# Optimization experiments

Hardware: AMD Instinct MI355X
Metric: run time of the kernel (lower is better)

Reference implementation:

```python
import jax, jax.numpy as jnp
import numpy as np

N = 120_000      # points
D = 64           # voxel grid resolution per axis
HID = 96         # hidden_dim
IN = 96          # input_dim
C = HID + IN     # 192, conv input channels
EPS = 1e-5       # BatchNorm eps


def _build_geometry(rng):
    """Precompute the hash-map lookups torchsparse builds on the fly."""
    pts = rng.uniform(0, D - 1e-3, size=(N, 3)).astype(np.float32)
    vox = np.floor(pts).astype(np.int64)                      # voxel coord per point
    flat = (vox[:, 0] * D + vox[:, 1]) * D + vox[:, 2]
    uniq, seg = np.unique(flat, return_inverse=True)          # occupied voxels
    M = uniq.shape[0]
    lut = -np.ones(D * D * D, dtype=np.int64)
    lut[uniq] = np.arange(M)
    ux, uy, uz = uniq // (D * D), (uniq // D) % D, uniq % D
    # 27 kernel offsets for the 3x3x3 sparse conv
    offs = np.array([(dx, dy, dz) for dx in (-1, 0, 1)
                     for dy in (-1, 0, 1) for dz in (-1, 0, 1)], dtype=np.int64)
    nx = ux[:, None] + offs[None, :, 0]
    ny = uy[:, None] + offs[None, :, 1]
    nz = uz[:, None] + offs[None, :, 2]
    ok = (nx >= 0) & (nx < D) & (ny >= 0) & (ny < D) & (nz >= 0) & (nz < D)
    nflat = (np.clip(nx, 0, D - 1) * D + np.clip(ny, 0, D - 1)) * D + np.clip(nz, 0, D - 1)
    nbr = np.where(ok, lut[nflat], -1)
    nbr = np.where(nbr < 0, M, nbr).astype(np.int32)          # row M = zero pad
    # 8 trilinear corners for devoxelization
    frac = pts - vox
    coffs = np.array([(a, b, c) for a in (0, 1) for b in (0, 1) for c in (0, 1)], dtype=np.int64)
    cx = vox[:, 0:1] + coffs[None, :, 0]
    cy = vox[:, 1:2] + coffs[None, :, 1]
    cz = vox[:, 2:3] + coffs[None, :, 2]
    okc = (cx < D) & (cy < D) & (cz < D)
    cflat = (np.clip(cx, 0, D - 1) * D + np.clip(cy, 0, D - 1)) * D + np.clip(cz, 0, D - 1)
    cidx = np.where(okc, lut[cflat], -1)
    w = np.ones((N, 8), dtype=np.float32)
    for k in range(8):
        for d in range(3):
            w[:, k] *= frac[:, d] if coffs[k, d] == 1 else (1.0 - frac[:, d])
    w = np.where(cidx >= 0, w, 0.0).astype(np.float32)        # missing voxel -> weight 0
    cidx = np.where(cidx < 0, M, cidx).astype(np.int32)
    return seg.astype(np.int32), nbr, cidx, w


def setup_inputs() -> dict:
    rng = np.random.default_rng(0)
    seg, nbr, cidx, cw = _build_geometry(rng)
    key = jax.random.key(0)
    ks = jax.random.split(key, 4)
    return {
        "hidden_F": jax.random.normal(ks[0], (N, HID), jnp.float32),
        "query_F": jax.random.normal(ks[1], (N, IN), jnp.float32),
        "W_conv": jax.random.normal(ks[2], (27, C, HID), jnp.float32) * (1.0 / np.sqrt(27.0 * C)),
        "gamma": jnp.ones((HID,), jnp.float32),
        "beta": jnp.zeros((HID,), jnp.float32),
        "W_lin": jax.random.normal(ks[3], (C, IN), jnp.float32) * (1.0 / np.sqrt(C)),
        "b_lin": jnp.zeros((IN,), jnp.float32),
        "corner_w": jnp.asarray(cw),
        "seg_ids": jnp.asarray(seg),
        "nbr_idx": jnp.asarray(nbr),
        "corner_idx": jnp.asarray(cidx),
    }


def reference(hidden_F, query_F, W_conv, gamma, beta, W_lin, b_lin, corner_w,
              seg_ids, nbr_idx, corner_idx):
    M = nbr_idx.shape[0]
    hx = jnp.concatenate([hidden_F, query_F], axis=1)                  # [N, C]
    # initial_voxelize: scatter-mean point features into occupied voxels
    vsum = jax.ops.segment_sum(hx, seg_ids, num_segments=M)            # [M, C]
    cnt = jax.ops.segment_sum(jnp.ones((hx.shape[0], 1), hx.dtype),
                              seg_ids, num_segments=M)
    vfeat = vsum / jnp.maximum(cnt, 1.0)
    # sparse 3x3x3 conv: gather 27 hashed neighbors (row M is zero pad)
    vpad = jnp.concatenate([vfeat, jnp.zeros((1, C), vfeat.dtype)], axis=0)
    acc = jnp.zeros((M, HID), vfeat.dtype)
    for k in range(27):  # fixed small kernel loop
        acc = acc + vpad[nbr_idx[:, k]] @ W_conv[k]
    # BatchNorm (batch stats over occupied voxels) + ReLU
    mu = jnp.mean(acc, axis=0)
    var = jnp.mean((acc - mu) ** 2, axis=0)
    y = jax.nn.relu(gamma * (acc - mu) * jax.lax.rsqrt(var + EPS) + beta)
    # voxel_to_point(nearest=False): trilinear 8-corner gather
    ypad = jnp.concatenate([y, jnp.zeros((1, HID), y.dtype)], axis=0)
    out = jnp.zeros((hx.shape[0], HID), y.dtype)
    for k in range(8):  # fixed corner loop
        out = out + corner_w[:, k:k + 1] * ypad[corner_idx[:, k]]
    # residual point transform: out.F + Linear(hx.F)
    return out + hx @ W_lin + b_lin
```

## Files before the change

### kernel.cpp

```cpp
#include <hip/hip_runtime.h>
#include <hip/hip_bf16.h>
#include <cstdint>

typedef __bf16 bf16;
typedef __bf16 bf16x8 __attribute__((ext_vector_type(8)));
typedef __bf16 bf16x4 __attribute__((ext_vector_type(4)));
typedef float f32x4 __attribute__((ext_vector_type(4)));
typedef int i32x4 __attribute__((ext_vector_type(4)));

#define HIDC 96
#define CINC 192
#define EPSC 1e-5f

#define STG_B 20480
#define STG_ELEM 10240

#define GLD_LDS16(g, l)                                                        \
  __builtin_amdgcn_global_load_lds(                                            \
      (const __attribute__((address_space(1))) void*)(g),                      \
      (__attribute__((address_space(3))) void*)(l), 16, 0, 0)

__global__ void k_repack(const float* __restrict__ Wc, const float* __restrict__ Wl,
                         bf16* __restrict__ dst, int total) {
  int t = blockIdx.x * 256 + threadIdx.x;
  if (t >= total) return;
  int off = t / 18432;
  int rem = t - off * 18432;
  int cix = rem >> 9;
  int lane = (rem >> 3) & 63;
  int j = rem & 7;
  int k = (cix / 6) * 32 + ((lane >> 4) << 3) + j;
  int col = (cix % 6) * 16 + (lane & 15);
  const float* src = (off < 27) ? (Wc + ((size_t)off * CINC + k) * HIDC + col)
                                : (Wl + (size_t)k * HIDC + col);
  int half = (cix >= 18) ? 1 : 0;
  size_t de = (size_t)(off * 2 + half) * STG_ELEM + (size_t)(rem - half * 9216);
  dst[de] = (bf16)(*src);
}

__global__ void k_count(const int* __restrict__ seg, int* __restrict__ cnt, int Npts) {
  int t = blockIdx.x * 256 + threadIdx.x;
  if (t < Npts) atomicAdd(cnt + seg[t], 1);
}

__global__ void k_bsum(const int* __restrict__ cnt, int* __restrict__ bsum, int M) {
  __shared__ int sm[256];
  int i = blockIdx.x * 256 + threadIdx.x;
  sm[threadIdx.x] = (i < M) ? cnt[i] : 0;
  __syncthreads();
  for (int st = 128; st > 0; st >>= 1) {
    if (threadIdx.x < st) sm[threadIdx.x] += sm[threadIdx.x + st];
    __syncthreads();
  }
  if (threadIdx.x == 0) bsum[blockIdx.x] = sm[0];
}

__global__ void k_bscan(int* __restrict__ bsum, int nb) {
  __shared__ int sm[1024];
  int i = threadIdx.x;
  int v = (i < nb) ? bsum[i] : 0;
  sm[i] = v;
  __syncthreads();
  for (int st = 1; st < 1024; st <<= 1) {
    int t = (i >= st) ? sm[i - st] : 0;
    __syncthreads();
    sm[i] += t;
    __syncthreads();
  }
  if (i < nb) bsum[i] = sm[i] - v;
}

__global__ void k_ptr(const int* __restrict__ cnt, const int* __restrict__ bsum,
                      int* __restrict__ ptr, int* __restrict__ cursor, int M) {
  __shared__ int sm[256];
  int i = blockIdx.x * 256 + threadIdx.x;
  int v = (i < M) ? cnt[i] : 0;
  sm[threadIdx.x] = v;
  __syncthreads();
  for (int st = 1; st < 256; st <<= 1) {
    int t = (threadIdx.x >= st) ? sm[threadIdx.x - st] : 0;
    __syncthreads();
    sm[threadIdx.x] += t;
    __syncthreads();
  }
  if (i < M) {
    int e = bsum[blockIdx.x] + sm[threadIdx.x] - v;
    ptr[i] = e;
    cursor[i] = e;
  }
}

__global__ void k_scatter(const int* __restrict__ seg, int* __restrict__ cursor,
                          int* __restrict__ plist, int Npts) {
  int t = blockIdx.x * 256 + threadIdx.x;
  if (t < Npts) {
    int pos = atomicAdd(cursor + seg[t], 1);
    plist[pos] = t;
  }
}

__global__ void k_gmean(const float* __restrict__ hid, const float* __restrict__ qry,
                        const int* __restrict__ ptr, const int* __restrict__ cnt,
                        const int* __restrict__ plist, bf16* __restrict__ vpad, int M) {
  int t = blockIdx.x * 256 + threadIdx.x;
  if (t >= (M + 1) * 48) return;
  int v = t / 48;
  int q = t - v * 48;
  f32x4 a = {0.f, 0.f, 0.f, 0.f};
  if (v < M) {
    int st = ptr[v], n = cnt[v];
    const float* base = (q < 24) ? (hid + q * 4) : (qry + (q - 24) * 4);
    for (int j = 0; j < n; j++) {
      int p = plist[st + j];
      a += *(const f32x4*)(base + (size_t)p * HIDC);
    }
    a *= (1.0f / (float)(n > 0 ? n : 1));
  }
  bf16x4 o;
#pragma unroll
  for (int j = 0; j < 4; j++) o[j] = (bf16)a[j];
  *(bf16x4*)(vpad + (size_t)v * CINC + q * 4) = o;
}

__launch_bounds__(128, 2)
__global__ void k_conv(const bf16* __restrict__ vpad, const int* __restrict__ nbr,
                       const bf16* __restrict__ wpack, float* __restrict__ accbuf,
                       float* __restrict__ bnsum, int M, int nblk, int nper) {
  const int bx = (int)(blockIdx.x & 7) * nper + (int)(blockIdx.x >> 3);
  if (bx >= nblk) return;
  __shared__ bf16 Bb[2][STG_B / 2];
  const int tid = threadIdx.x;
  const int wave = tid >> 6;
  const int lane = tid & 63;
  const int m = lane & 15;
  const int quad = lane >> 4;
  const int rb = bx * 128 + wave * 64;

  f32x4 acc[4][6];
#pragma unroll
  for (int rt = 0; rt < 4; rt++)
#pragma unroll
    for (int ct = 0; ct < 6; ct++) {
      f32x4 z = {0.f, 0.f, 0.f, 0.f};
      acc[rt][ct] = z;
    }

  const char* wb = (const char*)wpack;
  {
    char* dstb = (char*)&Bb[0][0];
#pragma unroll
    for (int i = 0; i < 10; i++) {
      const int base = (wave * 64 + i * 128) * 16;
      GLD_LDS16(wb + base + lane * 16, dstb + base);
    }
  }
  int gidx[4], gidx2[4];
#pragma unroll
  for (int rt = 0; rt < 4; rt++) {
    int r = rb + rt * 16 + m;
    gidx[rt] = (r < M) ? nbr[(size_t)r * 27] : M;
  }
  bf16x8 af[4][3];
#pragma unroll
  for (int kc2 = 0; kc2 < 3; kc2++)
#pragma unroll
    for (int rt = 0; rt < 4; rt++)
      af[rt][kc2] = *(const bf16x8*)(vpad + (size_t)gidx[rt] * CINC + kc2 * 32 + quad * 8);
  __syncthreads();

  for (int s = 0; s < 54; s++) {
    const int buf = s & 1;
    if (s < 53) {
      const char* src = wb + (size_t)(s + 1) * STG_B;
      char* dstb = (char*)&Bb[buf ^ 1][0];
#pragma unroll
      for (int i = 0; i < 10; i++) {
        const int base = (wave * 64 + i * 128) * 16;
        GLD_LDS16(src + base + lane * 16, dstb + base);
      }
    }
    const int half = s & 1;
    const int off = s >> 1;
    if (half == 0) {
      const int offn = off + 1;
#pragma unroll
      for (int rt = 0; rt < 4; rt++) {
        int r = rb + rt * 16 + m;
        gidx2[rt] = (r < M && offn < 27) ? nbr[(size_t)r * 27 + offn] : M;
      }
    }
    const char* bbr = (const char*)&Bb[buf][0];
#pragma unroll
    for (int kc2 = 0; kc2 < 3; kc2++) {
#pragma unroll
      for (int ct = 0; ct < 6; ct++) {
        bf16x8 bfm = *(const bf16x8*)(bbr + (size_t)(kc2 * 6 + ct) * 1024 + (size_t)lane * 16);
#pragma unroll
        for (int rt = 0; rt < 4; rt++)
          acc[rt][ct] = __builtin_amdgcn_mfma_f32_16x16x32_bf16(af[rt][kc2], bfm, acc[rt][ct], 0, 0, 0);
      }
      if (s < 53) {
        if (half == 0) {
#pragma unroll
          for (int rt = 0; rt < 4; rt++)
            af[rt][kc2] = *(const bf16x8*)(vpad + (size_t)gidx[rt] * CINC +
                                           (kc2 + 3) * 32 + quad * 8);
        } else {
#pragma unroll
          for (int rt = 0; rt < 4; rt++)
            af[rt][kc2] = *(const bf16x8*)(vpad + (size_t)gidx2[rt] * CINC +
                                           kc2 * 32 + quad * 8);
        }
      }
    }
    if (half == 1) {
#pragma unroll
      for (int rt = 0; rt < 4; rt++) gidx[rt] = gidx2[rt];
    }
    __syncthreads();
  }

  float ps[6], pq[6];
#pragma unroll
  for (int ct = 0; ct < 6; ct++) { ps[ct] = 0.f; pq[ct] = 0.f; }
#pragma unroll
  for (int rt = 0; rt < 4; rt++) {
#pragma unroll
    for (int rr = 0; rr < 4; rr++) {
      const int r2 = rb + rt * 16 + quad * 4 + rr;
      if (r2 < M) {
        float* dst = accbuf + (size_t)r2 * HIDC + m;
#pragma unroll
        for (int ct = 0; ct < 6; ct++) {
          float v = acc[rt][ct][rr];
          dst[ct * 16] = v;
          ps[ct] += v;
          pq[ct] += v * v;
        }
      }
    }
  }
#pragma unroll
  for (int ct = 0; ct < 6; ct++) {
    float s1 = ps[ct], s2 = pq[ct];
    s1 += __shfl_xor(s1, 16);
    s2 += __shfl_xor(s2, 16);
    s1 += __shfl_xor(s1, 32);
    s2 += __shfl_xor(s2, 32);
    if (quad == 0) {
      atomicAdd(bnsum + ct * 16 + m, s1);
      atomicAdd(bnsum + 96 + ct * 16 + m, s2);
    }
  }
}

__global__ void k_bnapply(const float* __restrict__ accbuf, const float* __restrict__ bnsum,
                          const float* __restrict__ gamma, const float* __restrict__ beta,
                          bf16* __restrict__ ypad, int M) {
  __shared__ float ssc[96], ssh[96];
  if (threadIdx.x < 96) {
    int c = threadIdx.x;
    float inv = 1.0f / (float)M;
    float mu = bnsum[c] * inv;
    float var = fmaxf(bnsum[96 + c] * inv - mu * mu, 0.f);
    float sc = gamma[c] * rsqrtf(var + EPSC);
    ssc[c] = sc;
    ssh[c] = beta[c] - mu * sc;
  }
  __syncthreads();
  int t = blockIdx.x * 256 + threadIdx.x;
  if (t >= (M + 1) * 24) return;
  int v = t / 24;
  int g = t - v * 24;
  f32x4 y = {0.f, 0.f, 0.f, 0.f};
  if (v < M) {
    f32x4 a = *(const f32x4*)(accbuf + (size_t)v * HIDC + g * 4);
#pragma unroll
    for (int j = 0; j < 4; j++) y[j] = fmaxf(a[j] * ssc[g * 4 + j] + ssh[g * 4 + j], 0.f);
  }
  bf16x4 o;
#pragma unroll
  for (int j = 0; j < 4; j++) o[j] = (bf16)y[j];
  *(bf16x4*)(ypad + (size_t)v * HIDC + g * 4) = o;
}

__launch_bounds__(256, 4)
__global__ void k_linear(const float* __restrict__ hid, const float* __restrict__ qry,
                         const bf16* __restrict__ wlpack, const float* __restrict__ blin,
                         bf16* __restrict__ lin, int Npts) {
  const int tid = threadIdx.x;
  const int wave = tid >> 6;
  const int lane = tid & 63;
  const int m = lane & 15;
  const int quad = lane >> 4;
  const int rb = blockIdx.x * 128 + wave * 32;

  f32x4 acc[2][6];
#pragma unroll
  for (int rt = 0; rt < 2; rt++)
#pragma unroll
    for (int ct = 0; ct < 6; ct++) {
      f32x4 z = {0.f, 0.f, 0.f, 0.f};
      acc[rt][ct] = z;
    }

  int prow[2];
#pragma unroll
  for (int rt = 0; rt < 2; rt++) {
    int r = rb + rt * 16 + m;
    prow[rt] = (r < Npts) ? r : (Npts - 1);
  }
  const char* wp = (const char*)wlpack;
#pragma unroll
  for (int kc = 0; kc < 6; kc++) {
    const float* srcA = (kc < 3) ? (hid + kc * 32) : (qry + (kc - 3) * 32);
    bf16x8 af[2];
#pragma unroll
    for (int rt = 0; rt < 2; rt++) {
      const float* pA = srcA + (size_t)prow[rt] * HIDC + quad * 8;
      f32x4 lo = *(const f32x4*)pA;
      f32x4 hi = *(const f32x4*)(pA + 4);
#pragma unroll
      for (int j = 0; j < 4; j++) {
        af[rt][j] = (bf16)lo[j];
        af[rt][4 + j] = (bf16)hi[j];
      }
    }
    const int half = (kc >= 3) ? 1 : 0;
    const int kcl = kc - half * 3;
#pragma unroll
    for (int ct = 0; ct < 6; ct++) {
      bf16x8 bfm = *(const bf16x8*)(wp + (size_t)half * STG_B +
                                    (size_t)((kcl * 6 + ct) * 64 + lane) * 16);
#pragma unroll
      for (int rt = 0; rt < 2; rt++)
        acc[rt][ct] = __builtin_amdgcn_mfma_f32_16x16x32_bf16(af[rt], bfm, acc[rt][ct], 0, 0, 0);
    }
  }
  float bl[6];
#pragma unroll
  for (int ct = 0; ct < 6; ct++) bl[ct] = blin[ct * 16 + m];
#pragma unroll
  for (int rt = 0; rt < 2; rt++)
#pragma unroll
    for (int rr = 0; rr < 4; rr++) {
      const int r2 = rb + rt * 16 + quad * 4 + rr;
      if (r2 < Npts) {
        bf16* dst = lin + (size_t)r2 * HIDC + m;
#pragma unroll
        for (int ct = 0; ct < 6; ct++)
          dst[ct * 16] = (bf16)(acc[rt][ct][rr] + bl[ct]);
      }
    }
}

__global__ void k_out(const bf16* __restrict__ lin, const bf16* __restrict__ ypad,
                      const float* __restrict__ cw, const int* __restrict__ cidx,
                      float* __restrict__ out, int Npts) {
  int t = blockIdx.x * 256 + threadIdx.x;
  if (t >= Npts * 12) return;
  int p = t / 12;
  int g = t - p * 12;
  float a[8];
  bf16x8 lv = *(const bf16x8*)(lin + (size_t)p * HIDC + g * 8);
#pragma unroll
  for (int j = 0; j < 8; j++) a[j] = (float)lv[j];
  f32x4 w0 = *(const f32x4*)(cw + (size_t)p * 8);
  f32x4 w1 = *(const f32x4*)(cw + (size_t)p * 8 + 4);
  const i32x4* cp = (const i32x4*)(cidx + (size_t)p * 8);
  i32x4 c0 = cp[0], c1 = cp[1];
#pragma unroll
  for (int k = 0; k < 8; k++) {
    int idx = (k < 4) ? c0[k] : c1[k - 4];
    float wk = (k < 4) ? w0[k] : w1[k - 4];
    bf16x8 yv = *(const bf16x8*)(ypad + (size_t)idx * HIDC + g * 8);
#pragma unroll
    for (int j = 0; j < 8; j++) a[j] += wk * (float)yv[j];
  }
  float* op = out + (size_t)p * HIDC + g * 8;
  f32x4 s0, s1;
#pragma unroll
  for (int j = 0; j < 4; j++) { s0[j] = a[j]; s1[j] = a[4 + j]; }
  *(f32x4*)op = s0;
  *(f32x4*)(op + 4) = s1;
}

extern "C" void kernel_launch(void* const* d_in, const int* in_sizes, int n_in,
                              void* d_out, int out_size, void* d_ws, size_t ws_size,
                              hipStream_t stream) {
  const float* hid = (const float*)d_in[0];
  const float* qry = (const float*)d_in[1];
  const float* Wc = (const float*)d_in[2];
  const float* gamma = (const float*)d_in[3];
  const float* beta = (const float*)d_in[4];
  const float* Wl = (const float*)d_in[5];
  const float* blin = (const float*)d_in[6];
  const float* cw = (const float*)d_in[7];
  const int* seg = (const int*)d_in[8];
  const int* nbr = (const int*)d_in[9];
  const int* cidx = (const int*)d_in[10];
  float* out = (float*)d_out;
  const int Npts = in_sizes[0] / HIDC;
  const int M = in_sizes[9] / 27;

  char* ws = (char*)d_ws;
  size_t cur = 0;
  auto alloc = [&](size_t b) { size_t o = cur; cur = (cur + b + 255) & ~(size_t)255; return o; };
  size_t o_cnt = alloc((size_t)M * 4);
  size_t o_bn = alloc(192 * 4);
  size_t zend = cur;
  size_t o_ptr = alloc((size_t)M * 4);
  size_t o_cur = alloc((size_t)M * 4);
  size_t o_pl = alloc((size_t)Npts * 4);
  size_t o_bs = alloc(1024 * 4);
  size_t RA = (size_t)M * HIDC * 4;
  size_t needA = (size_t)Npts * HIDC * 2;
  if (needA > RA) RA = needA;
  size_t o_A = alloc(RA);
  size_t o_B = alloc((size_t)(M + 1) * CINC * 2);
  size_t o_wpack = alloc((size_t)56 * STG_B);
  (void)ws_size; (void)n_in; (void)out_size;

  int* cnt = (int*)(ws + o_cnt);
  float* bnsum = (float*)(ws + o_bn);
  int* ptr = (int*)(ws + o_ptr);
  int* cursor = (int*)(ws + o_cur);
  int* plist = (int*)(ws + o_pl);
  int* bsum = (int*)(ws + o_bs);
  float* accbuf = (float*)(ws + o_A);
  bf16* lin = (bf16*)(ws + o_A);
  bf16* vpad = (bf16*)(ws + o_B);
  bf16* ypad = (bf16*)(ws + o_B);
  bf16* wpack = (bf16*)(ws + o_wpack);
  bf16* wlpack = (bf16*)(ws + o_wpack + (size_t)54 * STG_B);

  hipMemsetAsync(ws, 0, zend, stream);

  int totalRepack = 28 * 18432;
  k_repack<<<(totalRepack + 255) / 256, 256, 0, stream>>>(Wc, Wl, wpack, totalRepack);

  int nb = (M + 255) / 256;
  k_count<<<(Npts + 255) / 256, 256, 0, stream>>>(seg, cnt, Npts);
  k_bsum<<<nb, 256, 0, stream>>>(cnt, bsum, M);
  k_bscan<<<1, 1024, 0, stream>>>(bsum, nb);
  k_ptr<<<nb, 256, 0, stream>>>(cnt, bsum, ptr, cursor, M);
  k_scatter<<<(Npts + 255) / 256, 256, 0, stream>>>(seg, cursor, plist, Npts);
  k_gmean<<<(((M + 1) * 48) + 255) / 256, 256, 0, stream>>>(hid, qry, ptr, cnt, plist, vpad, M);

  int nblk = (M + 127) / 128;
  int nper = (nblk + 7) / 8;
  k_conv<<<nper * 8, 128, 0, stream>>>(vpad, nbr, wpack, accbuf, bnsum, M, nblk, nper);
  k_bnapply<<<((M + 1) * 24 + 255) / 256, 256, 0, stream>>>(accbuf, bnsum, gamma, beta, ypad, M);
  k_linear<<<(Npts + 127) / 128, 256, 0, stream>>>(hid, qry, wlpack, blin, lin, Npts);
  k_out<<<(Npts * 12 + 255) / 256, 256, 0, stream>>>(lin, ypad, cw, cidx, out, Npts);
}
```

Baseline: 396.4 us.

## Load conv weights directly into registers instead of LDS double-buffering

The conv kernel stops staging weight chunks in LDS through global_load_lds with double buffering and per-stage __syncthreads. Each wave now loads B fragments straight from global memory (expected to be L2-resident) into a register double buffer, prefetching the next cluster while MFMAs run. This removes LDS traffic and block barriers but costs more VGPRs and repeated global/L2 weight reads by every wave.

```diff
diff --git a/kernel.cpp b/kernel.cpp
--- a/kernel.cpp
+++ b/kernel.cpp
@@ -14,11 +14,6 @@
 
 #define STG_B 20480
 #define STG_ELEM 10240
-
-#define GLD_LDS16(g, l)                                                        \
-  __builtin_amdgcn_global_load_lds(                                            \
-      (const __attribute__((address_space(1))) void*)(g),                      \
-      (__attribute__((address_space(3))) void*)(l), 16, 0, 0)
 
 __global__ void k_repack(const float* __restrict__ Wc, const float* __restrict__ Wl,
                          bf16* __restrict__ dst, int total) {
@@ -128,7 +123,6 @@
                        float* __restrict__ bnsum, int M, int nblk, int nper) {
   const int bx = (int)(blockIdx.x & 7) * nper + (int)(blockIdx.x >> 3);
   if (bx >= nblk) return;
-  __shared__ bf16 Bb[2][STG_B / 2];
   const int tid = threadIdx.x;
   const int wave = tid >> 6;
   const int lane = tid & 63;
@@ -146,14 +140,8 @@
     }
 
   const char* wb = (const char*)wpack;
-  {
-    char* dstb = (char*)&Bb[0][0];
-#pragma unroll
-    for (int i = 0; i < 10; i++) {
-      const int base = (wave * 64 + i * 128) * 16;
-      GLD_LDS16(wb + base + lane * 16, dstb + base);
-    }
-  }
+  const size_t lane16 = (size_t)lane * 16;
+
   int gidx[4], gidx2[4];
 #pragma unroll
   for (int rt = 0; rt < 4; rt++) {
@@ -166,59 +154,63 @@
 #pragma unroll
     for (int rt = 0; rt < 4; rt++)
       af[rt][kc2] = *(const bf16x8*)(vpad + (size_t)gidx[rt] * CINC + kc2 * 32 + quad * 8);
-  __syncthreads();
-
-  for (int s = 0; s < 54; s++) {
-    const int buf = s & 1;
-    if (s < 53) {
-      const char* src = wb + (size_t)(s + 1) * STG_B;
-      char* dstb = (char*)&Bb[buf ^ 1][0];
-#pragma unroll
-      for (int i = 0; i < 10; i++) {
-        const int base = (wave * 64 + i * 128) * 16;
-        GLD_LDS16(src + base + lane * 16, dstb + base);
-      }
-    }
-    const int half = s & 1;
-    const int off = s >> 1;
-    if (half == 0) {
-      const int offn = off + 1;
-#pragma unroll
-      for (int rt = 0; rt < 4; rt++) {
-        int r = rb + rt * 16 + m;
-        gidx2[rt] = (r < M && offn < 27) ? nbr[(size_t)r * 27 + offn] : M;
-      }
-    }
-    const char* bbr = (const char*)&Bb[buf][0];
-#pragma unroll
-    for (int kc2 = 0; kc2 < 3; kc2++) {
-#pragma unroll
-      for (int ct = 0; ct < 6; ct++) {
-        bf16x8 bfm = *(const bf16x8*)(bbr + (size_t)(kc2 * 6 + ct) * 1024 + (size_t)lane * 16);
-#pragma unroll
-        for (int rt = 0; rt < 4; rt++)
-          acc[rt][ct] = __builtin_amdgcn_mfma_f32_16x16x32_bf16(af[rt][kc2], bfm, acc[rt][ct], 0, 0, 0);
-      }
-      if (s < 53) {
-        if (half == 0) {
-#pragma unroll
-          for (int rt = 0; rt < 4; rt++)
-            af[rt][kc2] = *(const bf16x8*)(vpad + (size_t)gidx[rt] * CINC +
-                                           (kc2 + 3) * 32 + quad * 8);
-        } else {
-#pragma unroll
-          for (int rt = 0; rt < 4; rt++)
-            af[rt][kc2] = *(const bf16x8*)(vpad + (size_t)gidx2[rt] * CINC +
-                                           kc2 * 32 + quad * 8);
-        }
-      }
-    }
-    if (half == 1) {
-#pragma unroll
-      for (int rt = 0; rt < 4; rt++) gidx[rt] = gidx2[rt];
-    }
-    __syncthreads();
-  }
+  bf16x8 bb[2][6];
+#pragma unroll
+  for (int ct = 0; ct < 6; ct++)
+    bb[0][ct] = *(const bf16x8*)(wb + (size_t)ct * 1024 + lane16);
+
+#define CLUSTER(CUR, S_N, K_N, NXT, K_C, PF)                                   \
+  {                                                                            \
+    if (PF) {                                                                  \
+      const char* bsrc = wb + (size_t)(S_N)*STG_B + (size_t)(K_N)*6144;        \
+      _Pragma("unroll")                                                        \
+      for (int ct = 0; ct < 6; ct++)                                           \
+        bb[NXT][ct] = *(const bf16x8*)(bsrc + (size_t)ct * 1024 + lane16);     \
+    }                                                                          \
+    _Pragma("unroll")                                                          \
+    for (int ct = 0; ct < 6; ct++)                                             \
+      _Pragma("unroll")                                                        \
+      for (int rt = 0; rt < 4; rt++)                                           \
+        acc[rt][ct] = __builtin_amdgcn_mfma_f32_16x16x32_bf16(                 \
+            af[rt][K_C], bb[CUR][ct], acc[rt][ct], 0, 0, 0);                   \
+  }
+
+  for (int off = 0; off < 27; off++) {
+    const int s0 = off * 2;
+    const int offn = off + 1;
+#pragma unroll
+    for (int rt = 0; rt < 4; rt++) {
+      int r = rb + rt * 16 + m;
+      gidx2[rt] = (r < M && offn < 27) ? nbr[(size_t)r * 27 + offn] : M;
+    }
+    CLUSTER(0, s0, 1, 1, 0, true);
+#pragma unroll
+    for (int rt = 0; rt < 4; rt++)
+      af[rt][0] = *(const bf16x8*)(vpad + (size_t)gidx[rt] * CINC + 3 * 32 + quad * 8);
+    CLUSTER(1, s0, 2, 0, 1, true);
+#pragma unroll
+    for (int rt = 0; rt < 4; rt++)
+      af[rt][1] = *(const bf16x8*)(vpad + (size_t)gidx[rt] * CINC + 4 * 32 + quad * 8);
+    CLUSTER(0, s0 + 1, 0, 1, 2, true);
+#pragma unroll
+    for (int rt = 0; rt < 4; rt++)
+      af[rt][2] = *(const bf16x8*)(vpad + (size_t)gidx[rt] * CINC + 5 * 32 + quad * 8);
+    CLUSTER(1, s0 + 1, 1, 0, 0, true);
+#pragma unroll
+    for (int rt = 0; rt < 4; rt++)
+      af[rt][0] = *(const bf16x8*)(vpad + (size_t)gidx2[rt] * CINC + 0 * 32 + quad * 8);
+    CLUSTER(0, s0 + 1, 2, 1, 1, true);
+#pragma unroll
+    for (int rt = 0; rt < 4; rt++)
+      af[rt][1] = *(const bf16x8*)(vpad + (size_t)gidx2[rt] * CINC + 1 * 32 + quad * 8);
+    CLUSTER(1, s0 + 2, 0, 0, 2, (off < 26));
+#pragma unroll
+    for (int rt = 0; rt < 4; rt++)
+      af[rt][2] = *(const bf16x8*)(vpad + (size_t)gidx2[rt] * CINC + 2 * 32 + quad * 8);
+#pragma unroll
+    for (int rt = 0; rt < 4; rt++) gidx[rt] = gidx2[rt];
+  }
+#undef CLUSTER
 
   float ps[6], pq[6];
 #pragma unroll
```

Result: slower. 450.2 us (+13.6%).

## Use 4 waves per conv block with split-barrier pipelining and LDS-staged stores

Applied to the files above, without the earlier changes.

The sparse conv kernel now runs 256 threads per 128-row tile, so each wave owns 32 rows instead of 64, which halves the accumulator registers and raises occupancy. The per-stage __syncthreads is replaced by an explicit vmcnt wait plus s_barrier, and the A fragments are double-buffered in registers so gathers overlap the MFMAs. The epilogue stages accumulators through LDS so rows are written to global memory as coalesced 16-byte stores. Each wave now reloads the shared weight stage for half as many rows, and the hand-written vmcnt count must match the number of loads in flight or results are wrong.

```diff
diff --git a/kernel.cpp b/kernel.cpp
--- a/kernel.cpp
+++ b/kernel.cpp
@@ -122,23 +122,23 @@
   *(bf16x4*)(vpad + (size_t)v * CINC + q * 4) = o;
 }
 
-__launch_bounds__(128, 2)
+__launch_bounds__(256, 4)
 __global__ void k_conv(const bf16* __restrict__ vpad, const int* __restrict__ nbr,
                        const bf16* __restrict__ wpack, float* __restrict__ accbuf,
                        float* __restrict__ bnsum, int M, int nblk, int nper) {
   const int bx = (int)(blockIdx.x & 7) * nper + (int)(blockIdx.x >> 3);
   if (bx >= nblk) return;
-  __shared__ bf16 Bb[2][STG_B / 2];
+  __shared__ __align__(16) char smem[40960];
   const int tid = threadIdx.x;
   const int wave = tid >> 6;
   const int lane = tid & 63;
   const int m = lane & 15;
   const int quad = lane >> 4;
-  const int rb = bx * 128 + wave * 64;
-
-  f32x4 acc[4][6];
-#pragma unroll
-  for (int rt = 0; rt < 4; rt++)
+  const int rb = bx * 128 + wave * 32;
+
+  f32x4 acc[2][6];
+#pragma unroll
+  for (int rt = 0; rt < 2; rt++)
 #pragma unroll
     for (int ct = 0; ct < 6; ct++) {
       f32x4 z = {0.f, 0.f, 0.f, 0.f};
@@ -146,100 +146,107 @@
     }
 
   const char* wb = (const char*)wpack;
+
   {
-    char* dstb = (char*)&Bb[0][0];
-#pragma unroll
-    for (int i = 0; i < 10; i++) {
-      const int base = (wave * 64 + i * 128) * 16;
+    char* dstb = smem;
+#pragma unroll
+    for (int i = 0; i < 5; i++) {
+      const int base = wave * 1024 + i * 4096;
       GLD_LDS16(wb + base + lane * 16, dstb + base);
     }
   }
-  int gidx[4], gidx2[4];
-#pragma unroll
-  for (int rt = 0; rt < 4; rt++) {
+  int gidx[2], gidx2[2];
+#pragma unroll
+  for (int rt = 0; rt < 2; rt++) {
     int r = rb + rt * 16 + m;
     gidx[rt] = (r < M) ? nbr[(size_t)r * 27] : M;
   }
-  bf16x8 af[4][3];
+  bf16x8 afn[2][3];
 #pragma unroll
   for (int kc2 = 0; kc2 < 3; kc2++)
 #pragma unroll
-    for (int rt = 0; rt < 4; rt++)
-      af[rt][kc2] = *(const bf16x8*)(vpad + (size_t)gidx[rt] * CINC + kc2 * 32 + quad * 8);
-  __syncthreads();
+    for (int rt = 0; rt < 2; rt++)
+      afn[rt][kc2] = *(const bf16x8*)(vpad + (size_t)gidx[rt] * CINC + kc2 * 32 + quad * 8);
+  __builtin_amdgcn_s_barrier();
 
   for (int s = 0; s < 54; s++) {
     const int buf = s & 1;
-    if (s < 53) {
-      const char* src = wb + (size_t)(s + 1) * STG_B;
-      char* dstb = (char*)&Bb[buf ^ 1][0];
-#pragma unroll
-      for (int i = 0; i < 10; i++) {
-        const int base = (wave * 64 + i * 128) * 16;
-        GLD_LDS16(src + base + lane * 16, dstb + base);
-      }
-    }
     const int half = s & 1;
     const int off = s >> 1;
     if (half == 0) {
       const int offn = off + 1;
 #pragma unroll
-      for (int rt = 0; rt < 4; rt++) {
+      for (int rt = 0; rt < 2; rt++) {
         int r = rb + rt * 16 + m;
         gidx2[rt] = (r < M && offn < 27) ? nbr[(size_t)r * 27 + offn] : M;
       }
     }
-    const char* bbr = (const char*)&Bb[buf][0];
+    if (s < 53) {
+      const char* src = wb + (size_t)(s + 1) * STG_B;
+      char* dstb = smem + (buf ^ 1) * STG_B;
+#pragma unroll
+      for (int i = 0; i < 5; i++) {
+        const int base = wave * 1024 + i * 4096;
+        GLD_LDS16(src + base + lane * 16, dstb + base);
+      }
+    }
+    __builtin_amdgcn_sched_barrier(0);
+
+    bf16x8 afc[2][3];
+#pragma unroll
+    for (int kc2 = 0; kc2 < 3; kc2++)
+#pragma unroll
+      for (int rt = 0; rt < 2; rt++) afc[rt][kc2] = afn[rt][kc2];
+
+    const char* bbr = smem + buf * STG_B;
 #pragma unroll
     for (int kc2 = 0; kc2 < 3; kc2++) {
 #pragma unroll
       for (int ct = 0; ct < 6; ct++) {
         bf16x8 bfm = *(const bf16x8*)(bbr + (size_t)(kc2 * 6 + ct) * 1024 + (size_t)lane * 16);
 #pragma unroll
-        for (int rt = 0; rt < 4; rt++)
-          acc[rt][ct] = __builtin_amdgcn_mfma_f32_16x16x32_bf16(af[rt][kc2], bfm, acc[rt][ct], 0, 0, 0);
+        for (int rt = 0; rt < 2; rt++)
+          acc[rt][ct] = __builtin_amdgcn_mfma_f32_16x16x32_bf16(afc[rt][kc2], bfm, acc[rt][ct], 0, 0, 0);
       }
       if (s < 53) {
         if (half == 0) {
 #pragma unroll
-          for (int rt = 0; rt < 4; rt++)
-            af[rt][kc2] = *(const bf16x8*)(vpad + (size_t)gidx[rt] * CINC +
-                                           (kc2 + 3) * 32 + quad * 8);
+          for (int rt = 0; rt < 2; rt++)
+            afn[rt][kc2] = *(const bf16x8*)(vpad + (size_t)gidx[rt] * CINC +
+                                            (kc2 + 3) * 32 + quad * 8);
         } else {
 #pragma unroll
-          for (int rt = 0; rt < 4; rt++)
-            af[rt][kc2] = *(const bf16x8*)(vpad + (size_t)gidx2[rt] * CINC +
-                                           kc2 * 32 + quad * 8);
+          for (int rt = 0; rt < 2; rt++)
+            afn[rt][kc2] = *(const bf16x8*)(vpad + (size_t)gidx2[rt] * CINC +
+                                            kc2 * 32 + quad * 8);
         }
       }
     }
     if (half == 1) {
-#pragma unroll
-      for (int rt = 0; rt < 4; rt++) gidx[rt] = gidx2[rt];
-    }
-    __syncthreads();
+      gidx[0] = gidx2[0];
+      gidx[1] = gidx2[1];
+    }
+    asm volatile("s_waitcnt vmcnt(6)" ::: "memory");
+    __builtin_amdgcn_s_barrier();
   }
 
   float ps[6], pq[6];
 #pragma unroll
   for (int ct = 0; ct < 6; ct++) { ps[ct] = 0.f; pq[ct] = 0.f; }
 #pragma unroll
-  for (int rt = 0; rt < 4; rt++) {
+  for (int rt = 0; rt < 2; rt++)
 #pragma unroll
     for (int rr = 0; rr < 4; rr++) {
       const int r2 = rb + rt * 16 + quad * 4 + rr;
       if (r2 < M) {
-        float* dst = accbuf + (size_t)r2 * HIDC + m;
 #pragma unroll
         for (int ct = 0; ct < 6; ct++) {
           float v = acc[rt][ct][rr];
-          dst[ct * 16] = v;
           ps[ct] += v;
           pq[ct] += v * v;
         }
       }
     }
-  }
 #pragma unroll
   for (int ct = 0; ct < 6; ct++) {
     float s1 = ps[ct], s2 = pq[ct];
@@ -250,6 +257,29 @@
     if (quad == 0) {
       atomicAdd(bnsum + ct * 16 + m, s1);
       atomicAdd(bnsum + 96 + ct * 16 + m, s2);
+    }
+  }
+  float(*trw)[98] = (float(*)[98])(smem + wave * (16 * 98 * 4));
+  const int erow = lane >> 3;
+  const int ecb = (lane & 7) * 4;
+#pragma unroll
+  for (int rt = 0; rt < 2; rt++) {
+#pragma unroll
+    for (int ct = 0; ct < 6; ct++)
+#pragma unroll
+      for (int rr = 0; rr < 4; rr++)
+        trw[quad * 4 + rr][ct * 16 + m] = acc[rt][ct][rr];
+#pragma unroll
+    for (int rh = 0; rh < 2; rh++) {
+      const int row = rh * 8 + erow;
+      const int r2 = rb + rt * 16 + row;
+      if (r2 < M) {
+#pragma unroll
+        for (int it = 0; it < 3; it++) {
+          f32x4 v = *(const f32x4*)&trw[row][it * 32 + ecb];
+          *(f32x4*)(accbuf + (size_t)r2 * HIDC + it * 32 + ecb) = v;
+        }
+      }
     }
   }
 }
@@ -449,7 +479,7 @@
 
   int nblk = (M + 127) / 128;
   int nper = (nblk + 7) / 8;
-  k_conv<<<nper * 8, 128, 0, stream>>>(vpad, nbr, wpack, accbuf, bnsum, M, nblk, nper);
+  k_conv<<<nper * 8, 256, 0, stream>>>(vpad, nbr, wpack, accbuf, bnsum, M, nblk, nper);
   k_bnapply<<<((M + 1) * 24 + 255) / 256, 256, 0, stream>>>(accbuf, bnsum, gamma, beta, ypad, M);
   k_linear<<<(Npts + 127) / 128, 256, 0, stream>>>(hid, qry, wlpack, blin, lin, Npts);
   k_out<<<(Npts * 12 + 255) / 256, 256, 0, stream>>>(lin, ypad, cw, cidx, out, Npts);
```

Measured after the change: 420.7 us. 6.1% more time.
